# Performance work log

Measured on AMD Instinct MI355X. Metric: run time of the kernel, lower is better.

The kernel has to match this reference:

```python
import jax, jax.numpy as jnp
import numpy as np

S = 4          # num_segments
T = 4096       # frames
D = 1024       # input_size == output_size
HEADS = 1
FREQ = 10000.0
DH = D // HEADS     # per-head width = 1024
TB = T // S         # block height = 1024
WB = DH // S        # block width  = 256


def _abs_pos(tb, d, freq):
    # Matches getAbsolutePosition: AP[p, 2i] = sin(p / freq^(2i/d)), AP[p, 2i+1] = cos(same).
    pos = jnp.arange(tb, dtype=jnp.float32)[:, None]          # [tb,1]
    i = jnp.arange(tb // 2, dtype=jnp.float32)[None, :]       # [1,tb//2]
    ang = pos / jnp.power(jnp.float32(freq), 2.0 * i / d)     # [tb,tb//2]
    ap = jnp.zeros((tb, tb), jnp.float32)
    return ap.at[:, 0::2].set(jnp.sin(ang)).at[:, 1::2].set(jnp.cos(ang))


def setup_inputs() -> dict:
    key = jax.random.key(0)
    ks = jax.random.split(key, 6)
    x = jax.random.normal(ks[0], (T, D), jnp.float32)
    Wq = jax.random.normal(ks[1], (HEADS, DH, D), jnp.float32) * 0.02
    Wk = jax.random.normal(ks[2], (HEADS, DH, D), jnp.float32) * 0.02
    Wv = jax.random.normal(ks[3], (HEADS, DH, D), jnp.float32) * 0.02
    Wout = jax.random.normal(ks[4], (D, D), jnp.float32) * 0.02
    Wout2 = jax.random.normal(ks[5], (WB, WB + 2), jnp.float32) * 0.05
    return {"x": x, "Wq": Wq, "Wk": Wk, "Wv": Wv, "Wout": Wout, "Wout2": Wout2}


def _forward(x, Wq, Wk, Wv, Wout, Wout2):
    # diversity = 1 - cosine similarity (F.normalize p=2 along dim=1)
    xu = x / jnp.maximum(jnp.linalg.norm(x, axis=1, keepdims=True), 1e-12)
    div = 1.0 - xu @ xu.T                                     # [T,T]

    Q = jnp.einsum('ti,hdi->htd', x, Wq)                      # [h,T,DH]
    K = jnp.einsum('ti,hdi->htd', x, Wk)
    V = jnp.einsum('ti,hdi->htd', x, Wv)

    def blk(A):  # [h,T,DH] -> [h,S*S,TB,WB], block (i,j) row-major as in local_x/local_y
        return A.reshape(-1, S, TB, S, WB).transpose(0, 1, 3, 2, 4).reshape(-1, S * S, TB, WB)

    qb, kb, vb = blk(Q), blk(K), blk(V)
    # diversity uses the diagonal row-block for every column-block j of row i
    drow = jnp.stack([div[i * TB:(i + 1) * TB, i * TB:(i + 1) * TB] for i in range(S)], 0)  # [S,TB,TB]
    db = jnp.repeat(drow, S, axis=0)[None]                    # [1,S*S,TB,TB]

    sim = jnp.einsum('hbqc,hbkc->hbqk', qb, kb) + _abs_pos(TB, D, FREQ)  # [h,S*S,TB,TB]
    attw = jax.nn.softmax(sim, axis=-1)
    # normalized row entropy, then L1-normalized (F.normalize p=1)
    ent = -(attw * jax.nn.log_softmax(sim, axis=-1)).sum(-1) / jnp.log(jnp.float32(TB))  # [h,S*S,TB]
    ent = ent / jnp.maximum(jnp.abs(ent).sum(-1, keepdims=True), 1e-12)

    dep = (db * attw).sum(-1) / db.sum(-1)                    # [h,S*S,TB]
    att_win = attw + dep[:, :, None, :] * attw                # dep_factor rows are identical
    ctx = jnp.einsum('hbqk,hbkc->hbqc', att_win, vb)          # [h,S*S,TB,WB]

    chars = jax.lax.stop_gradient(jnp.stack([ent, dep], axis=-1))  # [h,S*S,TB,2] (detach)
    y = jnp.concatenate([ctx, chars], axis=-1) @ Wout2.T      # [h,S*S,TB,WB]

    # reassemble grid of blocks back to [h,T,DH], concat heads, final projection
    y = y.reshape(-1, S, S, TB, WB).transpose(0, 1, 3, 2, 4).reshape(-1, T, DH)
    y = y.transpose(1, 0, 2).reshape(T, HEADS * DH)
    return y @ Wout.T                                         # [T,D]


def reference(x, Wq, Wk, Wv, Wout, Wout2):
    return _forward(x, Wq, Wk, Wv, Wout, Wout2)
```

## Files before the change

kernel.cpp:

```cpp
#include <hip/hip_runtime.h>
#include <hip/hip_bf16.h>

#define TT 4096
#define DD 1024
#define TBB 1024
#define WBB 256

typedef __attribute__((ext_vector_type(8))) _Float16 half8;
typedef __attribute__((ext_vector_type(4))) _Float16 half4;
typedef __attribute__((ext_vector_type(16))) float f32x16;

__device__ __forceinline__ unsigned short f2h(float v) {
  _Float16 h = (_Float16)v;
  return *reinterpret_cast<unsigned short*>(&h);
}
__device__ __forceinline__ float h2f(unsigned short u) {
  _Float16 h = *reinterpret_cast<_Float16*>(&u);
  return (float)h;
}

__device__ __forceinline__ void gl_lds16(const unsigned short* g, unsigned short* l) {
  __builtin_amdgcn_global_load_lds(
      (const __attribute__((address_space(1))) void*)(unsigned long long)(g),
      (__attribute__((address_space(3))) void*)(unsigned long long)(l),
      16, 0, 0);
}

__device__ __forceinline__ float waveSum(float v) {
#pragma unroll
  for (int o = 32; o > 0; o >>= 1) v += __shfl_down(v, o, 64);
  return v;
}
__device__ __forceinline__ float bSum(float v) {
#pragma unroll
  for (int o = 32; o > 0; o >>= 1) v += __shfl_xor(v, o, 64);
  return v;
}
__device__ __forceinline__ float bMax(float v) {
#pragma unroll
  for (int o = 32; o > 0; o >>= 1) v = fmaxf(v, __shfl_xor(v, o, 64));
  return v;
}

template <int EPI, typename OutT>
__global__ __launch_bounds__(256) void gemm_bt(
    const unsigned short* __restrict__ A, const unsigned short* __restrict__ B,
    OutT* __restrict__ C,
    int K, int lda, int ldb, int ldc,
    int zbase, int zdiv,
    long sAi, long sAj, long sBi, long sBj, long sCi, long sCj,
    long sAz, long sBz, long sCz,
    const float* __restrict__ e0, const float* __restrict__ e1,
    const float* __restrict__ e2, const float* __restrict__ e3)
{
  __shared__ __align__(16) unsigned short lA[2][4096];
  __shared__ __align__(16) unsigned short lB[2][4096];

  const int z = blockIdx.z, gz = zbase + z;
  const int zi = gz / zdiv, zj = gz - zi * zdiv;
  const unsigned short* Ab = A + (long)zi * sAi + (long)zj * sAj + (long)z * sAz;
  const unsigned short* Bb = B + (long)zi * sBi + (long)zj * sBj + (long)z * sBz;
  const long offC = (long)zi * sCi + (long)zj * sCj + (long)z * sCz;

  const int m0 = blockIdx.y * 128, n0 = blockIdx.x * 128;
  const int tid = threadIdx.x, wave = tid >> 6, lane = tid & 63;
  const int wm = (wave >> 1) * 64, wn = (wave & 1) * 64;
  const int srow = lane >> 2;
  const int scol = (((lane & 3) ^ ((srow >> 1) & 3))) * 8;
  const int l31 = lane & 31, khi = lane >> 5;
  const int sw2 = (l31 >> 1) & 3;

  f32x16 acc[2][2] = {};

  for (int k0 = 0; k0 < K; k0 += 64) {
#pragma unroll
    for (int h = 0; h < 2; ++h)
#pragma unroll
      for (int t = 0; t < 2; ++t) {
        const int r = wave * 32 + t * 16 + srow;
        gl_lds16(Ab + (long)(m0 + r) * lda + (k0 + h * 32 + scol), &lA[h][wave * 1024 + t * 512]);
        gl_lds16(Bb + (long)(n0 + r) * ldb + (k0 + h * 32 + scol), &lB[h][wave * 1024 + t * 512]);
      }
    __syncthreads();

    half8 af[2][4], bfr[2][4];
#pragma unroll
    for (int mi = 0; mi < 2; ++mi)
#pragma unroll
      for (int ks = 0; ks < 4; ++ks)
        af[mi][ks] = *(const half8*)&lA[ks >> 1][(wm + mi * 32 + l31) * 32 + ((((ks & 1) * 2 + khi) ^ sw2) * 8)];
#pragma unroll
    for (int ni = 0; ni < 2; ++ni)
#pragma unroll
      for (int ks = 0; ks < 4; ++ks)
        bfr[ni][ks] = *(const half8*)&lB[ks >> 1][(wn + ni * 32 + l31) * 32 + ((((ks & 1) * 2 + khi) ^ sw2) * 8)];

#pragma unroll
    for (int ks = 0; ks < 4; ++ks)
#pragma unroll
      for (int mi = 0; mi < 2; ++mi)
#pragma unroll
        for (int ni = 0; ni < 2; ++ni)
          acc[mi][ni] = __builtin_amdgcn_mfma_f32_32x32x16_f16(af[mi][ks], bfr[ni][ks], acc[mi][ni], 0, 0, 0);
    __syncthreads();
  }

  OutT* Cb = C + offC;
#pragma unroll
  for (int mi = 0; mi < 2; ++mi)
#pragma unroll
    for (int ni = 0; ni < 2; ++ni)
#pragma unroll
      for (int r = 0; r < 16; ++r) {
        const int row = m0 + wm + mi * 32 + khi * 4 + (r & 3) + 8 * (r >> 2);
        const int col = n0 + wn + ni * 32 + l31;
        float v = acc[mi][ni][r];
        const long ci = (long)row * ldc + col;
        if constexpr (sizeof(OutT) == 2) {
          Cb[ci] = (OutT)f2h(v);
        } else {
          Cb[ci] = v;
        }
      }
}

template <int EPI, typename OutT>
__global__ __launch_bounds__(256) void gemm_s(
    const unsigned short* __restrict__ A, const unsigned short* __restrict__ B,
    OutT* __restrict__ C,
    int K, int lda, int ldb, int ldc,
    int zbase, int zdiv,
    long sAi, long sAj, long sBi, long sBj, long sCi, long sCj,
    long sAz, long sBz, long sCz,
    const float* __restrict__ e0, const float* __restrict__ e1,
    const float* __restrict__ e2, const float* __restrict__ e3)
{
  __shared__ __align__(16) unsigned short lA[2][2048];
  __shared__ __align__(16) unsigned short lB[2][2048];

  const int z = blockIdx.z, gz = zbase + z;
  const int zi = gz / zdiv, zj = gz - zi * zdiv;
  const unsigned short* Ab = A + (long)zi * sAi + (long)zj * sAj + (long)z * sAz;
  const unsigned short* Bb = B + (long)zi * sBi + (long)zj * sBj + (long)z * sBz;
  const long offC = (long)zi * sCi + (long)zj * sCj + (long)z * sCz;

  const int m0 = blockIdx.y * 64, n0 = blockIdx.x * 64;
  const int tid = threadIdx.x, wave = tid >> 6, lane = tid & 63;
  const int wm = (wave >> 1) * 32, wn = (wave & 1) * 32;
  const int srow = lane >> 2;
  const int grow = wave * 16 + srow;
  const int scol = (((lane & 3) ^ ((grow >> 1) & 3))) * 8;
  const int l31 = lane & 31, khi = lane >> 5;
  const int sw2 = (l31 >> 1) & 3;

  f32x16 acc = {};

  for (int k0 = 0; k0 < K; k0 += 64) {
#pragma unroll
    for (int h = 0; h < 2; ++h) {
      gl_lds16(Ab + (long)(m0 + grow) * lda + (k0 + h * 32 + scol), &lA[h][wave * 512]);
      gl_lds16(Bb + (long)(n0 + grow) * ldb + (k0 + h * 32 + scol), &lB[h][wave * 512]);
    }
    __syncthreads();

    half8 af[4], bfr[4];
#pragma unroll
    for (int ks = 0; ks < 4; ++ks) {
      af[ks] = *(const half8*)&lA[ks >> 1][(wm + l31) * 32 + ((((ks & 1) * 2 + khi) ^ sw2) * 8)];
      bfr[ks] = *(const half8*)&lB[ks >> 1][(wn + l31) * 32 + ((((ks & 1) * 2 + khi) ^ sw2) * 8)];
    }
#pragma unroll
    for (int ks = 0; ks < 4; ++ks)
      acc = __builtin_amdgcn_mfma_f32_32x32x16_f16(af[ks], bfr[ks], acc, 0, 0, 0);
    __syncthreads();
  }

  OutT* Cb = C + offC;
#pragma unroll
  for (int r = 0; r < 16; ++r) {
    const int row = m0 + wm + khi * 4 + (r & 3) + 8 * (r >> 2);
    const int col = n0 + wn + l31;
    float v = acc[r];
    if constexpr (EPI == 1) v = 1.0f - v;
    if constexpr (EPI == 3)
      v += e0[(long)gz * 1024 + row] * e2[col] + e1[(long)gz * 1024 + row] * e3[col];
    const long ci = (long)row * ldc + col;
    if constexpr (sizeof(OutT) == 2) {
      Cb[ci] = (OutT)f2h(v);
    } else {
      Cb[ci] = v;
    }
  }
}

__global__ __launch_bounds__(256) void sim_gemm(
    const unsigned short* __restrict__ A, const unsigned short* __restrict__ B,
    unsigned short* __restrict__ C,
    const unsigned short* __restrict__ APh)
{
  __shared__ __align__(16) unsigned short lA[2][4096];
  __shared__ __align__(16) unsigned short lB[2][4096];

  const int gz = blockIdx.z;
  const int zi = gz >> 2, zj = gz & 3;
  const unsigned short* Ab = A + (long)zi * (TBB * DD) + zj * WBB;
  const unsigned short* Bb = B + (long)zi * (TBB * DD) + zj * WBB;
  unsigned short* Cb = C + (long)gz * TBB * TBB;

  const int m0 = blockIdx.y * 128, n0 = blockIdx.x * 128;
  const int tid = threadIdx.x, wave = tid >> 6, lane = tid & 63;
  const int wm = (wave >> 1) * 64, wn = (wave & 1) * 64;
  const int srow = lane >> 2;
  const int scol = ((lane & 3) ^ ((srow >> 1) & 3)) * 8;
  const int l31 = lane & 31, khi = lane >> 5;
  const int sw2 = (l31 >> 1) & 3;

  f32x16 acc[2][2] = {};

  for (int k0 = 0; k0 < WBB; k0 += 64) {
#pragma unroll
    for (int h = 0; h < 2; ++h)
#pragma unroll
      for (int t = 0; t < 2; ++t) {
        const int r = wave * 32 + t * 16 + srow;
        gl_lds16(Ab + (long)(m0 + r) * DD + (k0 + h * 32 + scol), &lA[h][wave * 1024 + t * 512]);
        gl_lds16(Bb + (long)(n0 + r) * DD + (k0 + h * 32 + scol), &lB[h][wave * 1024 + t * 512]);
      }
    __syncthreads();

    half8 af[2][4], bfr[2][4];
#pragma unroll
    for (int mi = 0; mi < 2; ++mi)
#pragma unroll
      for (int ks = 0; ks < 4; ++ks)
        af[mi][ks] = *(const half8*)&lA[ks >> 1][(wm + mi * 32 + l31) * 32 + ((((ks & 1) * 2 + khi) ^ sw2) * 8)];
#pragma unroll
    for (int ni = 0; ni < 2; ++ni)
#pragma unroll
      for (int ks = 0; ks < 4; ++ks)
        bfr[ni][ks] = *(const half8*)&lB[ks >> 1][(wn + ni * 32 + l31) * 32 + ((((ks & 1) * 2 + khi) ^ sw2) * 8)];

#pragma unroll
    for (int ks = 0; ks < 4; ++ks)
#pragma unroll
      for (int mi = 0; mi < 2; ++mi)
#pragma unroll
        for (int ni = 0; ni < 2; ++ni)
          acc[mi][ni] = __builtin_amdgcn_mfma_f32_32x32x16_f16(af[mi][ks], bfr[ni][ks], acc[mi][ni], 0, 0, 0);
    __syncthreads();
  }

#pragma unroll
  for (int mi = 0; mi < 2; ++mi)
#pragma unroll
    for (int ni = 0; ni < 2; ++ni)
#pragma unroll
      for (int r = 0; r < 16; ++r) {
        const int row = m0 + wm + mi * 32 + khi * 4 + (r & 3) + 8 * (r >> 2);
        const int col = n0 + wn + ni * 32 + l31;
        Cb[(long)row * TBB + col] = f2h(acc[mi][ni][r] + h2f(APh[(long)row * 1024 + col]));
      }
}

__global__ __launch_bounds__(256) void ctx_gemm_s(
    const unsigned short* __restrict__ simh, const float* __restrict__ dep,
    const float* __restrict__ Brow,
    const unsigned short* __restrict__ Vt, unsigned short* __restrict__ ctx)
{
  __shared__ __align__(16) unsigned short lA[2][2048];
  __shared__ __align__(16) unsigned short lB[2][2048];
  __shared__ __align__(16) unsigned short sDepH[1024];

  const int gz = blockIdx.z, zi = gz >> 2, zj = gz & 3;
  const int m0 = blockIdx.y * 64, n0 = blockIdx.x * 64;
  const int tid = threadIdx.x, wave = tid >> 6, lane = tid & 63;
  const int wm = (wave >> 1) * 32, wn = (wave & 1) * 32;
  const int srow = lane >> 2;
  const int grow = wave * 16 + srow;
  const int scol = ((lane & 3) ^ ((grow >> 1) & 3)) * 8;
  const int l31 = lane & 31, khi = lane >> 5;
  const int sw2 = (l31 >> 1) & 3;

#pragma unroll
  for (int p = 0; p < 4; ++p)
    sDepH[tid + p * 256] = f2h(1.f + dep[(long)gz * 1024 + tid + p * 256]);
  __syncthreads();

  const float B0 = Brow[(long)gz * 1024 + m0 + (tid >> 3)];
  const float B1 = Brow[(long)gz * 1024 + m0 + 32 + (tid >> 3)];

  const unsigned short* Ab = simh + (long)gz * TBB * TBB;
  const unsigned short* Bb = Vt + (long)(zj * 256) * TT + (long)zi * 1024;

  f32x16 acc = {};

  for (int k0 = 0; k0 < 1024; k0 += 64) {
#pragma unroll
    for (int h = 0; h < 2; ++h)
      gl_lds16(Bb + (long)(n0 + grow) * TT + (k0 + h * 32 + scol), &lB[h][wave * 512]);
#pragma unroll
    for (int h = 0; h < 2; ++h)
#pragma unroll
      for (int p = 0; p < 2; ++p) {
        const int idx = p * 1024 + tid * 4;
        const int row = idx >> 5, col = idx & 31;
        const ushort4 wv = *(const ushort4*)(Ab + (long)(m0 + row) * 1024 + k0 + h * 32 + col);
        const float Bp = p ? B1 : B0;
        half4 ev;
        ev.x = (_Float16)exp2f(fmaf(h2f(wv.x), 1.4426950408889634f, -Bp));
        ev.y = (_Float16)exp2f(fmaf(h2f(wv.y), 1.4426950408889634f, -Bp));
        ev.z = (_Float16)exp2f(fmaf(h2f(wv.z), 1.4426950408889634f, -Bp));
        ev.w = (_Float16)exp2f(fmaf(h2f(wv.w), 1.4426950408889634f, -Bp));
        const half4 dv = *(const half4*)&sDepH[k0 + h * 32 + col];
        half4 pv = ev * dv;
        const int pcol = (((col >> 3) ^ ((row >> 1) & 3)) << 3) | (col & 7);
        *(half4*)&lA[h][row * 32 + pcol] = pv;
      }
    __syncthreads();

    half8 af[4], bfr[4];
#pragma unroll
    for (int ks = 0; ks < 4; ++ks) {
      af[ks] = *(const half8*)&lA[ks >> 1][(wm + l31) * 32 + ((((ks & 1) * 2 + khi) ^ sw2) * 8)];
      bfr[ks] = *(const half8*)&lB[ks >> 1][(wn + l31) * 32 + ((((ks & 1) * 2 + khi) ^ sw2) * 8)];
    }
#pragma unroll
    for (int ks = 0; ks < 4; ++ks)
      acc = __builtin_amdgcn_mfma_f32_32x32x16_f16(af[ks], bfr[ks], acc, 0, 0, 0);
    __syncthreads();
  }

  unsigned short* Cb = ctx + (long)gz * TBB * WBB;
#pragma unroll
  for (int r = 0; r < 16; ++r) {
    const int row = m0 + wm + khi * 4 + (r & 3) + 8 * (r >> 2);
    const int col = n0 + wn + l31;
    Cb[(long)row * WBB + col] = f2h(acc[r]);
  }
}

__global__ __launch_bounds__(256) void prepx_kernel(
    const float* __restrict__ x, unsigned short* __restrict__ xh,
    unsigned short* __restrict__ xu)
{
  const int t = blockIdx.x, tid = threadIdx.x;
  const float4 v = *((const float4*)(x + (long)t * DD) + tid);
  float ss = v.x * v.x + v.y * v.y + v.z * v.z + v.w * v.w;
  ss = waveSum(ss);
  __shared__ float red[4];
  if ((tid & 63) == 0) red[tid >> 6] = ss;
  __syncthreads();
  const float tot = red[0] + red[1] + red[2] + red[3];
  const float inv = 1.f / fmaxf(sqrtf(tot), 1e-12f);
  ushort4 h, u;
  h.x = f2h(v.x); h.y = f2h(v.y); h.z = f2h(v.z); h.w = f2h(v.w);
  u.x = f2h(v.x * inv); u.y = f2h(v.y * inv); u.z = f2h(v.z * inv); u.w = f2h(v.w * inv);
  *((ushort4*)(xh + (long)t * DD) + tid) = h;
  *((ushort4*)(xu + (long)t * DD) + tid) = u;
}

__global__ __launch_bounds__(256) void castall_kernel(
    const float* __restrict__ Wq, const float* __restrict__ Wk,
    const float* __restrict__ Wv, const float* __restrict__ Wo,
    unsigned short* __restrict__ Wh, unsigned short* __restrict__ WoB)
{
  const long idx4 = ((long)blockIdx.x * 256 + threadIdx.x) * 4;
  const int which = (int)(idx4 >> 20);
  const long loc = idx4 & ((1L << 20) - 1);
  const float* src = (which == 0) ? Wq : ((which == 1) ? Wk : ((which == 2) ? Wv : Wo));
  unsigned short* dst = (which < 3) ? (Wh + idx4) : (WoB + loc);
  const float4 v = *(const float4*)(src + loc);
  ushort4 h;
  h.x = f2h(v.x); h.y = f2h(v.y); h.z = f2h(v.z); h.w = f2h(v.w);
  *(ushort4*)dst = h;
}

__global__ __launch_bounds__(256) void packw2_kernel(
    const float* __restrict__ W2, unsigned short* __restrict__ W2B,
    float* __restrict__ Ecol, float* __restrict__ Dcol)
{
  const int c = blockIdx.x, j = threadIdx.x;
  W2B[c * 256 + j] = f2h(W2[c * 258 + j]);
  if (j == 0) {
    Ecol[c] = W2[c * 258 + 256];
    Dcol[c] = W2[c * 258 + 257];
  }
}

__global__ __launch_bounds__(256) void ap_kernel(unsigned short* __restrict__ APh)
{
  const int p = blockIdx.x, tid = threadIdx.x;
#pragma unroll
  for (int t = 0; t < 4; ++t) {
    const int col = tid + t * 256;
    const int i = col >> 1;
    const float e = (2.0f * (float)i) / 1024.0f;
    const float ang = (float)p * exp2f(e * -13.287712379549449f);
    APh[(long)p * 1024 + col] = f2h((col & 1) ? cosf(ang) : sinf(ang));
  }
}

__global__ __launch_bounds__(256) void transpose_kernel(
    const unsigned short* __restrict__ V, unsigned short* __restrict__ Vt)
{
  __shared__ unsigned short tile[32][33];
  const int tx = threadIdx.x & 31, ty = threadIdx.x >> 5;
  const int c0 = blockIdx.x * 32;
  const int r0 = blockIdx.y * 32;
#pragma unroll
  for (int rr = ty; rr < 32; rr += 8)
    tile[rr][tx] = V[(long)(r0 + rr) * DD + c0 + tx];
  __syncthreads();
#pragma unroll
  for (int rr = ty; rr < 32; rr += 8)
    Vt[(long)(c0 + rr) * TT + r0 + tx] = tile[tx][rr];
}

__global__ __launch_bounds__(256) void stats_kernel(
    const unsigned short* __restrict__ sim, const unsigned short* __restrict__ divb,
    float* __restrict__ dep, float* __restrict__ ent,
    float* __restrict__ Brow)
{
  const int gz = blockIdx.y, bi = gz >> 2;
  const int wave = threadIdx.x >> 6, lane = threadIdx.x & 63;
  const int q = blockIdx.x * 4 + wave;
  const unsigned short* srow = sim + ((long)gz * TBB + q) * TBB;
  const unsigned short* drow = divb + ((long)bi * TBB + q) * TBB;
  float s[16], d[16];
#pragma unroll
  for (int u = 0; u < 4; ++u) {
    const ushort4 sv = *(const ushort4*)(srow + u * 256 + lane * 4);
    const ushort4 dv = *(const ushort4*)(drow + u * 256 + lane * 4);
    s[u * 4 + 0] = h2f(sv.x); s[u * 4 + 1] = h2f(sv.y);
    s[u * 4 + 2] = h2f(sv.z); s[u * 4 + 3] = h2f(sv.w);
    d[u * 4 + 0] = h2f(dv.x); d[u * 4 + 1] = h2f(dv.y);
    d[u * 4 + 2] = h2f(dv.z); d[u * 4 + 3] = h2f(dv.w);
  }
  float m = s[0];
#pragma unroll
  for (int i = 1; i < 16; ++i) m = fmaxf(m, s[i]);
  m = bMax(m);
  const float mB = m * 1.4426950408889634f;
  float l = 0.f, ss = 0.f, dn = 0.f, ds = 0.f;
#pragma unroll
  for (int i = 0; i < 16; ++i) {
    const float e = exp2f(fmaf(s[i], 1.4426950408889634f, -mB));
    l += e; ss += e * s[i]; dn += e * d[i]; ds += d[i];
  }
  l = bSum(l); ss = bSum(ss); dn = bSum(dn); ds = bSum(ds);
  if (lane == 0) {
    const long o = (long)gz * TBB + q;
    const float Li = 1.f / l;
    const float lnL = logf(l);
    dep[o] = (dn * Li) / ds;
    ent[o] = (m + lnL - ss * Li) * 0.14426950408889634f;
    Brow[o] = (m + lnL) * 1.4426950408889634f;
  }
}

__global__ __launch_bounds__(256) void entnorm_kernel(float* __restrict__ ent)
{
  const int gz = blockIdx.x, tid = threadIdx.x;
  float s = 0.f;
#pragma unroll
  for (int p = 0; p < 4; ++p) s += fabsf(ent[(long)gz * TBB + tid + p * 256]);
  s = waveSum(s);
  __shared__ float red[4];
  if ((tid & 63) == 0) red[tid >> 6] = s;
  __syncthreads();
  const float scale = 1.f / fmaxf(red[0] + red[1] + red[2] + red[3], 1e-12f);
#pragma unroll
  for (int p = 0; p < 4; ++p) ent[(long)gz * TBB + tid + p * 256] *= scale;
}

extern "C" void kernel_launch(void* const* d_in, const int* in_sizes, int n_in,
                              void* d_out, int out_size, void* d_ws, size_t ws_size,
                              hipStream_t stream)
{
  const float* x  = (const float*)d_in[0];
  const float* Wq = (const float*)d_in[1];
  const float* Wk = (const float*)d_in[2];
  const float* Wv = (const float*)d_in[3];
  const float* Wo = (const float*)d_in[4];
  const float* W2 = (const float*)d_in[5];

  char* ws = (char*)d_ws;
  size_t off = 0;
  auto take = [&](size_t bytes) -> void* {
    void* p = ws + off;
    off += (bytes + 255) & ~(size_t)255;
    return p;
  };
  unsigned short* QKV = (unsigned short*)take((size_t)3 * TT * DD * 2);
  unsigned short* xh  = (unsigned short*)take((size_t)TT * DD * 2);
  unsigned short* xu  = (unsigned short*)take((size_t)TT * DD * 2);
  unsigned short* Wh  = (unsigned short*)take((size_t)3 * DD * DD * 2);
  unsigned short* WoB = (unsigned short*)take((size_t)DD * DD * 2);
  unsigned short* W2B = (unsigned short*)take((size_t)256 * 256 * 2);
  float* Ecol = (float*)take(256 * 4);
  float* Dcol = (float*)take(256 * 4);
  unsigned short* APh = (unsigned short*)take((size_t)TBB * TBB * 2);
  unsigned short* divb = (unsigned short*)take((size_t)4 * TBB * TBB * 2);
  unsigned short* Vt = (unsigned short*)take((size_t)DD * TT * 2);
  unsigned short* simh = (unsigned short*)take((size_t)16 * TBB * TBB * 2);
  float* depb = (float*)take((size_t)16 * TBB * 4);
  float* entb = (float*)take((size_t)16 * TBB * 4);
  float* Brow = (float*)take((size_t)16 * TBB * 4);
  unsigned short* ctx = (unsigned short*)take((size_t)16 * TBB * WBB * 2);
  unsigned short* Y = (unsigned short*)take((size_t)TT * DD * 2);
  (void)ws_size; (void)in_sizes; (void)n_in; (void)out_size;

  prepx_kernel<<<TT, 256, 0, stream>>>(x, xh, xu);
  castall_kernel<<<(4 * DD * DD) / 1024, 256, 0, stream>>>(Wq, Wk, Wv, Wo, Wh, WoB);
  packw2_kernel<<<256, 256, 0, stream>>>(W2, W2B, Ecol, Dcol);
  ap_kernel<<<TBB, 256, 0, stream>>>(APh);

  gemm_bt<0, unsigned short><<<dim3(DD / 128, TT / 128, 3), 256, 0, stream>>>(
      xh, Wh, QKV,
      DD, DD, DD, DD, 0, 1,
      0, 0, (long)DD * DD, 0, (long)TT * DD, 0,
      0, 0, 0, nullptr, nullptr, nullptr, nullptr);

  transpose_kernel<<<dim3(DD / 32, TT / 32), 256, 0, stream>>>(QKV + (size_t)2 * TT * DD, Vt);

  gemm_s<1, unsigned short><<<dim3(16, 16, 4), 256, 0, stream>>>(
      xu, xu, divb,
      DD, DD, DD, TBB, 0, 1,
      (long)TBB * DD, 0, (long)TBB * DD, 0, (long)TBB * TBB, 0,
      0, 0, 0, nullptr, nullptr, nullptr, nullptr);

  const unsigned short* Qh = QKV;
  const unsigned short* Kh = QKV + (size_t)TT * DD;

  sim_gemm<<<dim3(8, 8, 16), 256, 0, stream>>>(Qh, Kh, simh, APh);

  stats_kernel<<<dim3(TBB / 4, 16), 256, 0, stream>>>(simh, divb, depb, entb, Brow);
  entnorm_kernel<<<16, 256, 0, stream>>>(entb);

  ctx_gemm_s<<<dim3(4, 16, 16), 256, 0, stream>>>(simh, depb, Brow, Vt, ctx);

  gemm_s<3, unsigned short><<<dim3(4, 16, 16), 256, 0, stream>>>(
      ctx, W2B, Y,
      WBB, WBB, WBB, DD, 0, 4,
      (long)4 * TBB * WBB, (long)TBB * WBB, 0, 0, (long)TBB * DD, (long)WBB,
      0, 0, 0, entb, depb, Ecol, Dcol);

  gemm_s<0, float><<<dim3(16, 64, 1), 256, 0, stream>>>(
      Y, WoB, (float*)d_out,
      DD, DD, DD, DD, 0, 1,
      0, 0, 0, 0, 0, 0,
      0, 0, 0, nullptr, nullptr, nullptr, nullptr);
}
```

Baseline: 251.5 us.

## Compute V transposed directly and exploit symmetry of diversity GEMM

V is no longer produced by the QKV GEMM and then transposed; a separate GEMM computes Vt = Wv·xᵀ directly, which removes the transpose kernel and one round trip of V through memory. The diversity GEMM (xu·xuᵀ) now skips tiles below the diagonal and writes each off-diagonal tile's mirror through an LDS-staged transpose, roughly halving that GEMM's MFMA work. In exchange, the V projection runs on the smaller 64x64-tile kernel, and the mirrored tiles add extra syncs and stores.

```diff
diff --git a/kernel.cpp b/kernel.cpp
--- a/kernel.cpp
+++ b/kernel.cpp
@@ -138,6 +138,10 @@
   __shared__ __align__(16) unsigned short lA[2][2048];
   __shared__ __align__(16) unsigned short lB[2][2048];
 
+  if constexpr (EPI == 2) {
+    if (blockIdx.x < blockIdx.y) return;
+  }
+
   const int z = blockIdx.z, gz = zbase + z;
   const int zi = gz / zdiv, zj = gz - zi * zdiv;
   const unsigned short* Ab = A + (long)zi * sAi + (long)zj * sAj + (long)z * sAz;
@@ -181,7 +185,7 @@
     const int row = m0 + wm + khi * 4 + (r & 3) + 8 * (r >> 2);
     const int col = n0 + wn + l31;
     float v = acc[r];
-    if constexpr (EPI == 1) v = 1.0f - v;
+    if constexpr (EPI == 1 || EPI == 2) v = 1.0f - v;
     if constexpr (EPI == 3)
       v += e0[(long)gz * 1024 + row] * e2[col] + e1[(long)gz * 1024 + row] * e3[col];
     const long ci = (long)row * ldc + col;
@@ -189,6 +193,31 @@
       Cb[ci] = (OutT)f2h(v);
     } else {
       Cb[ci] = v;
+    }
+  }
+
+  if constexpr (EPI == 2) {
+    if (blockIdx.x != blockIdx.y) {
+      unsigned short* mir = &lA[0][0];
+      const int lc = wn + l31;
+#pragma unroll
+      for (int chunk = 0; chunk < 2; ++chunk) {
+        __syncthreads();
+        if ((lc >> 5) == chunk) {
+#pragma unroll
+          for (int r = 0; r < 16; ++r) {
+            const int lr = wm + khi * 4 + (r & 3) + 8 * (r >> 2);
+            mir[(lc & 31) * 68 + lr] = f2h(1.0f - acc[r]);
+          }
+        }
+        __syncthreads();
+        const int cl = tid >> 3, co = (tid & 7) * 8;
+        const ushort4 a = *(const ushort4*)&mir[cl * 68 + co];
+        const ushort4 b = *(const ushort4*)&mir[cl * 68 + co + 4];
+        unsigned short* dst = (unsigned short*)Cb + (long)(n0 + chunk * 32 + cl) * ldc + m0 + co;
+        *(ushort4*)dst = a;
+        *(ushort4*)(dst + 4) = b;
+      }
     }
   }
 }
@@ -400,22 +429,6 @@
   }
 }
 
-__global__ __launch_bounds__(256) void transpose_kernel(
-    const unsigned short* __restrict__ V, unsigned short* __restrict__ Vt)
-{
-  __shared__ unsigned short tile[32][33];
-  const int tx = threadIdx.x & 31, ty = threadIdx.x >> 5;
-  const int c0 = blockIdx.x * 32;
-  const int r0 = blockIdx.y * 32;
-#pragma unroll
-  for (int rr = ty; rr < 32; rr += 8)
-    tile[rr][tx] = V[(long)(r0 + rr) * DD + c0 + tx];
-  __syncthreads();
-#pragma unroll
-  for (int rr = ty; rr < 32; rr += 8)
-    Vt[(long)(c0 + rr) * TT + r0 + tx] = tile[tx][rr];
-}
-
 __global__ __launch_bounds__(256) void stats_kernel(
     const unsigned short* __restrict__ sim, const unsigned short* __restrict__ divb,
     float* __restrict__ dep, float* __restrict__ ent,
@@ -491,7 +504,7 @@
     off += (bytes + 255) & ~(size_t)255;
     return p;
   };
-  unsigned short* QKV = (unsigned short*)take((size_t)3 * TT * DD * 2);
+  unsigned short* QKV = (unsigned short*)take((size_t)2 * TT * DD * 2);
   unsigned short* xh  = (unsigned short*)take((size_t)TT * DD * 2);
   unsigned short* xu  = (unsigned short*)take((size_t)TT * DD * 2);
   unsigned short* Wh  = (unsigned short*)take((size_t)3 * DD * DD * 2);
@@ -515,15 +528,19 @@
   packw2_kernel<<<256, 256, 0, stream>>>(W2, W2B, Ecol, Dcol);
   ap_kernel<<<TBB, 256, 0, stream>>>(APh);
 
-  gemm_bt<0, unsigned short><<<dim3(DD / 128, TT / 128, 3), 256, 0, stream>>>(
+  gemm_bt<0, unsigned short><<<dim3(DD / 128, TT / 128, 2), 256, 0, stream>>>(
       xh, Wh, QKV,
       DD, DD, DD, DD, 0, 1,
       0, 0, (long)DD * DD, 0, (long)TT * DD, 0,
       0, 0, 0, nullptr, nullptr, nullptr, nullptr);
 
-  transpose_kernel<<<dim3(DD / 32, TT / 32), 256, 0, stream>>>(QKV + (size_t)2 * TT * DD, Vt);
-
-  gemm_s<1, unsigned short><<<dim3(16, 16, 4), 256, 0, stream>>>(
+  gemm_s<0, unsigned short><<<dim3(TT / 64, DD / 64, 1), 256, 0, stream>>>(
+      Wh + (size_t)2 * DD * DD, xh, Vt,
+      DD, DD, DD, TT, 0, 1,
+      0, 0, 0, 0, 0, 0,
+      0, 0, 0, nullptr, nullptr, nullptr, nullptr);
+
+  gemm_s<2, unsigned short><<<dim3(16, 16, 4), 256, 0, stream>>>(
       xu, xu, divb,
       DD, DD, DD, TBB, 0, 1,
       (long)TBB * DD, 0, (long)TBB * DD, 0, (long)TBB * TBB, 0,
```

After: 251.9 us. About the same (+0.1%).
